# Kernel tuning notes

Hardware: AMD Instinct MI355X
Metric: run time of the kernel (lower is better)

## Reference

```python
import jax, jax.numpy as jnp
import numpy as np

N_NODES = 50000
N_EDGES = 800000
IN_DIM, HID_DIM, OUT_DIM = 512, 64, 40


def setup_inputs() -> dict:
    key = jax.random.key(0)
    k1, k2, k3, k4, k5 = jax.random.split(key, 5)
    x = jax.random.normal(k1, (N_NODES, IN_DIM), dtype=jnp.float32)
    src = jax.random.randint(k2, (N_EDGES,), 0, N_NODES, dtype=jnp.int64)
    dst = jax.random.randint(k3, (N_EDGES,), 0, N_NODES, dtype=jnp.int64)
    # Linear weights stored as [in, out] (equivalent to torch W.T), no bias.
    W1 = jax.random.normal(k4, (IN_DIM, HID_DIM), dtype=jnp.float32) * (1.0 / np.sqrt(IN_DIM))
    W2 = jax.random.normal(k5, (HID_DIM, OUT_DIM), dtype=jnp.float32) * (1.0 / np.sqrt(HID_DIM))
    return {"x": x, "src": src, "dst": dst, "W1": W1, "W2": W2}


def _gnn_layer(x, src, dst, W, n_nodes):
    # linear projection then sparse-adjacency aggregation:
    # out[i] = sum_{(j->i) in E} (x @ W)[j]
    h = x @ W                                   # [N, out_dim]
    return jax.ops.segment_sum(h[src], dst, num_segments=n_nodes)


def reference(x, src, dst, W1, W2):
    n = x.shape[0]
    h = _gnn_layer(x, src, dst, W1, n)          # [N, HID]
    h = jax.nn.relu(h)
    h = _gnn_layer(h, src, dst, W2, n)          # [N, OUT]
    return jax.nn.log_softmax(h, axis=1)
```

## Files before the change

kernel.cpp:

```cpp
#include <hip/hip_runtime.h>
#include <hip/hip_bf16.h>
#include <math.h>

constexpr int IN_DIM = 512;
constexpr int HID = 64;
constexpr int OUTD = 40;
constexpr int CAP = 64;

typedef __attribute__((ext_vector_type(8))) short bf16x8;
typedef __attribute__((ext_vector_type(4))) float floatx4;
typedef unsigned short ushort_t;

__device__ __forceinline__ unsigned short f2bf(float f) {
    unsigned u = __float_as_uint(f);
    u += 0x7fff + ((u >> 16) & 1);
    return (unsigned short)(u >> 16);
}

__device__ __forceinline__ unsigned pk2(float x, float y) {
    __hip_bfloat162 h = __float22bfloat162_rn(make_float2(x, y));
    return *reinterpret_cast<unsigned*>(&h);
}

#define GW4 asm volatile("s_waitcnt vmcnt(4)" ::: "memory")
#define GW0 asm volatile("s_waitcnt vmcnt(0)" ::: "memory")

__global__ __launch_bounds__(256) void prep_kernel(const float* __restrict__ W1,
                                                   const float* __restrict__ W2,
                                                   ushort_t* __restrict__ Wt,
                                                   ushort_t* __restrict__ W2tb,
                                                   int* __restrict__ deg, int N) {
    int bid = blockIdx.x;
    if (bid < 128) {
        int tid = bid * 256 + threadIdx.x;
        int k = tid >> 6;
        int n = tid & 63;
        Wt[(size_t)((k >> 5) * 64 + n) * 32 + (k & 31)] = f2bf(W1[tid]);
    } else if (bid == 128) {
        for (int idx = threadIdx.x; idx < 3072; idx += 256) {
            int j = idx & 7;
            int l = (idx >> 3) & 63;
            int f = idx >> 9;
            int nt = f >> 1, ks = f & 1;
            int k = ks * 32 + (l >> 4) * 8 + j;
            int col = nt * 16 + (l & 15);
            float v = (col < OUTD) ? W2[k * OUTD + col] : 0.f;
            W2tb[idx] = f2bf(v);
        }
    } else {
        int i = (bid - 129) * 1024 + (int)threadIdx.x * 4;
        if (i + 3 < N) {
            *(int4*)&deg[i] = make_int4(0, 0, 0, 0);
        } else {
            for (int t = 0; t < 4; ++t)
                if (i + t < N) deg[i + t] = 0;
        }
    }
}

__global__ __launch_bounds__(256) void gemm1_fill_kernel(const float* __restrict__ x,
                                                         const ushort_t* __restrict__ Wt,
                                                         ushort_t* __restrict__ h1b,
                                                         const int* __restrict__ src,
                                                         const int* __restrict__ dst,
                                                         int* __restrict__ deg,
                                                         int* __restrict__ srcs,
                                                         int E, int N, int nSlices) {
    __shared__ char lds[4 * 2 * 4096];
    const int bid = blockIdx.x;
    const int grp = bid / 72;
    const int rem = bid - grp * 72;

    if (rem >= 8) {
        const int fidx = grp * 64 + rem - 8;
        if (fidx >= 8 * nSlices) return;
        const int part = fidx & 7;
        const int slice = fidx >> 3;
        const int PART = (N + 7) >> 3;
        const int lo = part * PART;
        const int hi = lo + PART;
        int e0 = (slice * 256 + (int)threadIdx.x) * 4;
        if (e0 + 3 < E) {
            int4 s4 = *(const int4*)&src[e0];
            int4 d4 = *(const int4*)&dst[e0];
            int p;
            if (d4.x >= lo && d4.x < hi) {
                p = atomicAdd(&deg[d4.x], 1); if (p < CAP) srcs[(d4.x << 6) + p] = s4.x;
            }
            if (d4.y >= lo && d4.y < hi) {
                p = atomicAdd(&deg[d4.y], 1); if (p < CAP) srcs[(d4.y << 6) + p] = s4.y;
            }
            if (d4.z >= lo && d4.z < hi) {
                p = atomicAdd(&deg[d4.z], 1); if (p < CAP) srcs[(d4.z << 6) + p] = s4.z;
            }
            if (d4.w >= lo && d4.w < hi) {
                p = atomicAdd(&deg[d4.w], 1); if (p < CAP) srcs[(d4.w << 6) + p] = s4.w;
            }
        } else {
            for (int i = 0; i < 4; ++i) {
                int e = e0 + i;
                if (e < E) {
                    int d = dst[e];
                    if (d >= lo && d < hi) {
                        int p = atomicAdd(&deg[d], 1);
                        if (p < CAP) srcs[(d << 6) + p] = src[e];
                    }
                }
            }
        }
        return;
    }

    const int gb = grp * 8 + rem;
    if (gb * 64 >= N) return;

    const int lane = threadIdx.x & 63;
    const int wave = threadIdx.x >> 6;
    const int lm = lane & 15;
    const int quad = lane >> 4;

    const int row0 = gb * 64 + wave * 16;
    char* wbase = lds + wave * 8192;
    char* b0 = wbase;
    char* b1 = wbase + 4096;

    const ushort_t* wB = Wt + lm * 32 + quad * 8;

    floatx4 acc0 = {0.f, 0.f, 0.f, 0.f};
    floatx4 acc1 = {0.f, 0.f, 0.f, 0.f};
    floatx4 acc2 = {0.f, 0.f, 0.f, 0.f};
    floatx4 acc3 = {0.f, 0.f, 0.f, 0.f};

    auto stage_chunk = [&](int c, char* buf) {
#pragma unroll
        for (int i = 0; i < 4; ++i) {
            int rr = i * 4 + (lane >> 4);
            int gr = row0 + rr;
            if (gr > N - 1) gr = N - 1;
            int g = (lane & 15) ^ (rr & 15);
            const float* gp = x + (size_t)gr * IN_DIM + c * 64 + g * 4;
            __builtin_amdgcn_global_load_lds((const void*)gp, (void*)(buf + i * 1024), 16, 0, 2);
        }
    };

    const int sz = (lm & 15) << 4;

    auto iter = [&](int c, const char* rbuf, char* sbuf, bool dostage, bool wait0) {
        if (dostage) stage_chunk(c + 1, sbuf);
        if (wait0) { GW0; } else { GW4; }
        const ushort_t* wc0 = wB + (size_t)(c * 2) * 2048;
        const ushort_t* wc1 = wc0 + 2048;
        bf16x8 bA0 = *(const bf16x8*)(wc0);
        bf16x8 bA1 = *(const bf16x8*)(wc0 + 512);
        bf16x8 bA2 = *(const bf16x8*)(wc0 + 1024);
        bf16x8 bA3 = *(const bf16x8*)(wc0 + 1536);
        bf16x8 bB0 = *(const bf16x8*)(wc1);
        bf16x8 bB1 = *(const bf16x8*)(wc1 + 512);
        bf16x8 bB2 = *(const bf16x8*)(wc1 + 1024);
        bf16x8 bB3 = *(const bf16x8*)(wc1 + 1536);
        const char* rp = rbuf + lm * 256;
        {
            float4 a0 = *(const float4*)(rp + (((quad * 2) << 4) ^ sz));
            float4 a1 = *(const float4*)(rp + (((quad * 2 + 1) << 4) ^ sz));
            union { bf16x8 v; unsigned u[4]; } af;
            af.u[0] = pk2(a0.x, a0.y);
            af.u[1] = pk2(a0.z, a0.w);
            af.u[2] = pk2(a1.x, a1.y);
            af.u[3] = pk2(a1.z, a1.w);
            acc0 = __builtin_amdgcn_mfma_f32_16x16x32_bf16(af.v, bA0, acc0, 0, 0, 0);
            acc1 = __builtin_amdgcn_mfma_f32_16x16x32_bf16(af.v, bA1, acc1, 0, 0, 0);
            acc2 = __builtin_amdgcn_mfma_f32_16x16x32_bf16(af.v, bA2, acc2, 0, 0, 0);
            acc3 = __builtin_amdgcn_mfma_f32_16x16x32_bf16(af.v, bA3, acc3, 0, 0, 0);
        }
        {
            float4 a0 = *(const float4*)(rp + (((8 + quad * 2) << 4) ^ sz));
            float4 a1 = *(const float4*)(rp + (((8 + quad * 2 + 1) << 4) ^ sz));
            union { bf16x8 v; unsigned u[4]; } af;
            af.u[0] = pk2(a0.x, a0.y);
            af.u[1] = pk2(a0.z, a0.w);
            af.u[2] = pk2(a1.x, a1.y);
            af.u[3] = pk2(a1.z, a1.w);
            acc0 = __builtin_amdgcn_mfma_f32_16x16x32_bf16(af.v, bB0, acc0, 0, 0, 0);
            acc1 = __builtin_amdgcn_mfma_f32_16x16x32_bf16(af.v, bB1, acc1, 0, 0, 0);
            acc2 = __builtin_amdgcn_mfma_f32_16x16x32_bf16(af.v, bB2, acc2, 0, 0, 0);
            acc3 = __builtin_amdgcn_mfma_f32_16x16x32_bf16(af.v, bB3, acc3, 0, 0, 0);
        }
    };

    stage_chunk(0, b0);

    iter(0, b0, b1, true, false);
    iter(1, b1, b0, true, false);
    iter(2, b0, b1, true, false);
    iter(3, b1, b0, true, false);
    iter(4, b0, b1, true, false);
    iter(5, b1, b0, true, false);
    iter(6, b0, b1, true, false);
    iter(7, b1, b0, false, true);

    const int rb = row0 + quad * 4;
#pragma unroll
    for (int reg = 0; reg < 4; ++reg) {
        int r = rb + reg;
        if (r < N) {
            ushort_t* hr = h1b + (size_t)r * HID + lm;
            hr[0]  = f2bf(acc0[reg]);
            hr[16] = f2bf(acc1[reg]);
            hr[32] = f2bf(acc2[reg]);
            hr[48] = f2bf(acc3[reg]);
        }
    }
}

template <int RELU>
__global__ __launch_bounds__(256) void agg_kernel(const ushort_t* __restrict__ hin,
                                                  const int* __restrict__ deg,
                                                  const int* __restrict__ srcs,
                                                  ushort_t* __restrict__ hout, int N) {
    int node = (blockIdx.x * 256 + threadIdx.x) >> 6;
    int lane = threadIdx.x & 63;
    if (node >= N) return;
    int dg = deg[node];
    if (dg > CAP) dg = CAP;
    int b = node << 6;
    int e = b + dg;
    const int half = lane >> 5;
    const int cp = lane & 31;
    float acc0 = 0.f, acc1 = 0.f;
    for (int j = b; j < e; j += 16) {
        int i0 = j + half * 8;
        int4 sa = *(const int4*)&srcs[i0];
        int4 sb = *(const int4*)&srcs[i0 + 4];
        int ss[8] = {sa.x, sa.y, sa.z, sa.w, sb.x, sb.y, sb.z, sb.w};
        unsigned u[8] = {0u, 0u, 0u, 0u, 0u, 0u, 0u, 0u};
#pragma unroll
        for (int t = 0; t < 8; ++t)
            if (i0 + t < e) u[t] = *(const unsigned*)&hin[(size_t)ss[t] * HID + cp * 2];
#pragma unroll
        for (int t = 0; t < 8; ++t) {
            acc0 += __uint_as_float(u[t] << 16);
            acc1 += __uint_as_float(u[t] & 0xffff0000u);
        }
    }
    acc0 += __shfl_xor(acc0, 32, 64);
    acc1 += __shfl_xor(acc1, 32, 64);
    if (half == 0) {
        float r0 = RELU ? fmaxf(acc0, 0.f) : acc0;
        float r1 = RELU ? fmaxf(acc1, 0.f) : acc1;
        *(unsigned*)&hout[(size_t)node * HID + cp * 2] = pk2(r0, r1);
    }
}

__global__ __launch_bounds__(256) void gemmlsm_kernel(const ushort_t* __restrict__ agg2b,
                                                      const ushort_t* __restrict__ W2tb,
                                                      float* __restrict__ out, int N) {
    const int lane = threadIdx.x & 63;
    const int wave = threadIdx.x >> 6;
    const int lm = lane & 15;
    const int quad = lane >> 4;
    const int row0 = (blockIdx.x * 4 + wave) * 16;

    int ar = row0 + lm;
    if (ar > N - 1) ar = N - 1;
    const ushort_t* ap = agg2b + (size_t)ar * HID + quad * 8;
    bf16x8 a0 = *(const bf16x8*)(ap);
    bf16x8 a1 = *(const bf16x8*)(ap + 32);

    const ushort_t* bp = W2tb + (size_t)lane * 8;
    bf16x8 b00 = *(const bf16x8*)(bp);
    bf16x8 b01 = *(const bf16x8*)(bp + 512);
    bf16x8 b10 = *(const bf16x8*)(bp + 1024);
    bf16x8 b11 = *(const bf16x8*)(bp + 1536);
    bf16x8 b20 = *(const bf16x8*)(bp + 2048);
    bf16x8 b21 = *(const bf16x8*)(bp + 2560);

    floatx4 c0 = {0.f, 0.f, 0.f, 0.f};
    floatx4 c1 = {0.f, 0.f, 0.f, 0.f};
    floatx4 c2 = {0.f, 0.f, 0.f, 0.f};
    c0 = __builtin_amdgcn_mfma_f32_16x16x32_bf16(a0, b00, c0, 0, 0, 0);
    c0 = __builtin_amdgcn_mfma_f32_16x16x32_bf16(a1, b01, c0, 0, 0, 0);
    c1 = __builtin_amdgcn_mfma_f32_16x16x32_bf16(a0, b10, c1, 0, 0, 0);
    c1 = __builtin_amdgcn_mfma_f32_16x16x32_bf16(a1, b11, c1, 0, 0, 0);
    c2 = __builtin_amdgcn_mfma_f32_16x16x32_bf16(a0, b20, c2, 0, 0, 0);
    c2 = __builtin_amdgcn_mfma_f32_16x16x32_bf16(a1, b21, c2, 0, 0, 0);

#pragma unroll
    for (int r = 0; r < 4; ++r) {
        float v0 = c0[r], v1 = c1[r], v2 = c2[r];
        float m = fmaxf(v0, v1);
        if (lm < 8) m = fmaxf(m, v2);
#pragma unroll
        for (int o = 8; o; o >>= 1) m = fmaxf(m, __shfl_xor(m, o, 64));
        float ex = expf(v0 - m) + expf(v1 - m) + ((lm < 8) ? expf(v2 - m) : 0.f);
#pragma unroll
        for (int o = 8; o; o >>= 1) ex += __shfl_xor(ex, o, 64);
        float ls = logf(ex);
        int row = row0 + quad * 4 + r;
        if (row < N) {
            float* orow = out + (size_t)row * OUTD;
            orow[lm] = v0 - m - ls;
            orow[16 + lm] = v1 - m - ls;
            if (lm < 8) orow[32 + lm] = v2 - m - ls;
        }
    }
}

extern "C" void kernel_launch(void* const* d_in, const int* in_sizes, int n_in,
                              void* d_out, int out_size, void* d_ws, size_t ws_size,
                              hipStream_t stream) {
    const float* x  = (const float*)d_in[0];
    const int*  src = (const int*)d_in[1];
    const int*  dst = (const int*)d_in[2];
    const float* W1 = (const float*)d_in[3];
    const float* W2 = (const float*)d_in[4];
    float* out = (float*)d_out;

    const int N = in_sizes[0] / IN_DIM;
    const int E = in_sizes[1];

    char* base = (char*)d_ws;
    ushort_t* Wt    = (ushort_t*)base;
    ushort_t* W2tb  = (ushort_t*)(base + 65536);
    ushort_t* h1b   = (ushort_t*)(base + 65536 + 8192);
    ushort_t* agg1b = h1b + (size_t)N * HID;
    ushort_t* agg2b = agg1b + (size_t)N * HID;
    int*   deg      = (int*)(agg2b + (size_t)N * HID);
    int*   srcs     = deg + N;

    const int degZeroBlocks = (N + 1023) / 1024;
    prep_kernel<<<129 + degZeroBlocks, 256, 0, stream>>>(W1, W2, Wt, W2tb, deg, N);

    const int nSlices = (E + 1023) / 1024;
    const int nGemmB = (N + 63) / 64;
    int nGroups = (nSlices * 8 + 63) / 64;
    int g2 = (nGemmB + 7) / 8;
    if (g2 > nGroups) nGroups = g2;
    gemm1_fill_kernel<<<nGroups * 72, 256, 0, stream>>>(x, Wt, h1b, src, dst, deg, srcs,
                                                        E, N, nSlices);

    agg_kernel<1><<<(N * 64 + 255) / 256, 256, 0, stream>>>(h1b, deg, srcs, agg1b, N);
    agg_kernel<0><<<(N * 64 + 255) / 256, 256, 0, stream>>>(agg1b, deg, srcs, agg2b, N);
    gemmlsm_kernel<<<(N + 63) / 64, 256, 0, stream>>>(agg2b, W2tb, out, N);
}
```

Baseline: 254.4 us.

## Pad neighbor lists with zero-row sentinel to remove per-edge bounds checks in aggregation

Prefills the CSR-like srcs slots with a sentinel index N that points at an appended all-zero row in h1b and agg1b, so unused slots contribute zero. The aggregation kernel then issues 16 unconditional gathers per half-wave up front and a second batch only when degree exceeds 32, instead of a degree-bounded loop with per-element predicates. This exposes more memory-level parallelism in the gather. In exchange it adds a large extra fill of N*64 ints in prep_kernel and always gathers at least 32 rows per node (mostly the sentinel row) even though the average degree is about 16.

```diff
diff --git a/kernel.cpp b/kernel.cpp
--- a/kernel.cpp
+++ b/kernel.cpp
@@ -29,8 +29,12 @@
                                                    const float* __restrict__ W2,
                                                    ushort_t* __restrict__ Wt,
                                                    ushort_t* __restrict__ W2tb,
-                                                   int* __restrict__ deg, int N) {
+                                                   int* __restrict__ deg,
+                                                   int* __restrict__ srcs,
+                                                   ushort_t* __restrict__ h1b,
+                                                   ushort_t* __restrict__ agg1b, int N) {
     int bid = blockIdx.x;
+    const int degZ = (N + 1023) >> 10;
     if (bid < 128) {
         int tid = bid * 256 + threadIdx.x;
         int k = tid >> 6;
@@ -47,13 +51,30 @@
             float v = (col < OUTD) ? W2[k * OUTD + col] : 0.f;
             W2tb[idx] = f2bf(v);
         }
-    } else {
+        if (threadIdx.x < 32)
+            ((unsigned*)(h1b + (size_t)N * HID))[threadIdx.x] = 0u;
+        else if (threadIdx.x < 64)
+            ((unsigned*)(agg1b + (size_t)N * HID))[threadIdx.x - 32] = 0u;
+    } else if (bid < 129 + degZ) {
         int i = (bid - 129) * 1024 + (int)threadIdx.x * 4;
         if (i + 3 < N) {
             *(int4*)&deg[i] = make_int4(0, 0, 0, 0);
         } else {
             for (int t = 0; t < 4; ++t)
                 if (i + t < N) deg[i + t] = 0;
+        }
+    } else {
+        int i = (bid - 129 - degZ) * 4096 + (int)threadIdx.x * 16;
+        const int total = N * CAP;
+        int4 sv = make_int4(N, N, N, N);
+        if (i + 15 < total) {
+            *(int4*)&srcs[i] = sv;
+            *(int4*)&srcs[i + 4] = sv;
+            *(int4*)&srcs[i + 8] = sv;
+            *(int4*)&srcs[i + 12] = sv;
+        } else {
+            for (int t = 0; t < 16; ++t)
+                if (i + t < total) srcs[i + t] = N;
         }
     }
 }
@@ -217,27 +238,48 @@
                                                   const int* __restrict__ deg,
                                                   const int* __restrict__ srcs,
                                                   ushort_t* __restrict__ hout, int N) {
-    int node = (blockIdx.x * 256 + threadIdx.x) >> 6;
+    int node = blockIdx.x * 4 + (threadIdx.x >> 6);
     int lane = threadIdx.x & 63;
     if (node >= N) return;
-    int dg = deg[node];
-    if (dg > CAP) dg = CAP;
-    int b = node << 6;
-    int e = b + dg;
     const int half = lane >> 5;
     const int cp = lane & 31;
+    const int b = node << 6;
+
+    int i0 = b + half * 16;
+    int4 sa = *(const int4*)&srcs[i0];
+    int4 sb = *(const int4*)&srcs[i0 + 4];
+    int4 sc = *(const int4*)&srcs[i0 + 8];
+    int4 sd = *(const int4*)&srcs[i0 + 12];
+    int dg = deg[node];
+
     float acc0 = 0.f, acc1 = 0.f;
-    for (int j = b; j < e; j += 16) {
-        int i0 = j + half * 8;
-        int4 sa = *(const int4*)&srcs[i0];
-        int4 sb = *(const int4*)&srcs[i0 + 4];
-        int ss[8] = {sa.x, sa.y, sa.z, sa.w, sb.x, sb.y, sb.z, sb.w};
-        unsigned u[8] = {0u, 0u, 0u, 0u, 0u, 0u, 0u, 0u};
-#pragma unroll
-        for (int t = 0; t < 8; ++t)
-            if (i0 + t < e) u[t] = *(const unsigned*)&hin[(size_t)ss[t] * HID + cp * 2];
-#pragma unroll
-        for (int t = 0; t < 8; ++t) {
+    {
+        int ss[16] = {sa.x, sa.y, sa.z, sa.w, sb.x, sb.y, sb.z, sb.w,
+                      sc.x, sc.y, sc.z, sc.w, sd.x, sd.y, sd.z, sd.w};
+        unsigned u[16];
+#pragma unroll
+        for (int t = 0; t < 16; ++t)
+            u[t] = *(const unsigned*)&hin[(size_t)ss[t] * HID + cp * 2];
+#pragma unroll
+        for (int t = 0; t < 16; ++t) {
+            acc0 += __uint_as_float(u[t] << 16);
+            acc1 += __uint_as_float(u[t] & 0xffff0000u);
+        }
+    }
+    if (dg > 32) {
+        int j0 = i0 + 32;
+        int4 ta = *(const int4*)&srcs[j0];
+        int4 tb = *(const int4*)&srcs[j0 + 4];
+        int4 tc = *(const int4*)&srcs[j0 + 8];
+        int4 td = *(const int4*)&srcs[j0 + 12];
+        int ss[16] = {ta.x, ta.y, ta.z, ta.w, tb.x, tb.y, tb.z, tb.w,
+                      tc.x, tc.y, tc.z, tc.w, td.x, td.y, td.z, td.w};
+        unsigned u[16];
+#pragma unroll
+        for (int t = 0; t < 16; ++t)
+            u[t] = *(const unsigned*)&hin[(size_t)ss[t] * HID + cp * 2];
+#pragma unroll
+        for (int t = 0; t < 16; ++t) {
             acc0 += __uint_as_float(u[t] << 16);
             acc1 += __uint_as_float(u[t] & 0xffff0000u);
         }
@@ -322,13 +364,15 @@
     ushort_t* Wt    = (ushort_t*)base;
     ushort_t* W2tb  = (ushort_t*)(base + 65536);
     ushort_t* h1b   = (ushort_t*)(base + 65536 + 8192);
-    ushort_t* agg1b = h1b + (size_t)N * HID;
-    ushort_t* agg2b = agg1b + (size_t)N * HID;
+    ushort_t* agg1b = h1b + (size_t)(N + 1) * HID;
+    ushort_t* agg2b = agg1b + (size_t)(N + 1) * HID;
     int*   deg      = (int*)(agg2b + (size_t)N * HID);
     int*   srcs     = deg + N;
 
-    const int degZeroBlocks = (N + 1023) / 1024;
-    prep_kernel<<<129 + degZeroBlocks, 256, 0, stream>>>(W1, W2, Wt, W2tb, deg, N);
+    const int degZ = (N + 1023) >> 10;
+    const int fillB = (N * CAP + 4095) / 4096;
+    prep_kernel<<<129 + degZ + fillB, 256, 0, stream>>>(W1, W2, Wt, W2tb, deg, srcs,
+                                                        h1b, agg1b, N);
 
     const int nSlices = (E + 1023) / 1024;
     const int nGemmB = (N + 63) / 64;
@@ -338,7 +382,7 @@
     gemm1_fill_kernel<<<nGroups * 72, 256, 0, stream>>>(x, Wt, h1b, src, dst, deg, srcs,
                                                         E, N, nSlices);
 
-    agg_kernel<1><<<(N * 64 + 255) / 256, 256, 0, stream>>>(h1b, deg, srcs, agg1b, N);
-    agg_kernel<0><<<(N * 64 + 255) / 256, 256, 0, stream>>>(agg1b, deg, srcs, agg2b, N);
+    agg_kernel<1><<<(N + 3) / 4, 256, 0, stream>>>(h1b, deg, srcs, agg1b, N);
+    agg_kernel<0><<<(N + 3) / 4, 256, 0, stream>>>(agg1b, deg, srcs, agg2b, N);
     gemmlsm_kernel<<<(N + 63) / 64, 256, 0, stream>>>(agg2b, W2tb, out, N);
 }
```

Result: faster. 236.2 us (-7.2%).
